# Kernel tuning notes

Hardware: AMD Instinct MI355X
Metric: run time of the kernel (lower is better)

The kernel has to match this reference:

```python
import jax, jax.numpy as jnp
import numpy as np

INPUT_SIZE = 1024
OUTPUT_SIZE = 1024
BLOCK_SIZE = 60
T = 4096
EPS = 1e-12


def setup_inputs() -> dict:
    key = jax.random.key(0)
    k1, k2, k3, k4, k5 = jax.random.split(key, 5)
    s_in = 1.0 / np.sqrt(INPUT_SIZE)
    s_out = 1.0 / np.sqrt(OUTPUT_SIZE + 2)
    return {
        "x": jax.random.normal(k1, (T, INPUT_SIZE), dtype=jnp.float32),
        "Wk": jax.random.normal(k2, (OUTPUT_SIZE, INPUT_SIZE), dtype=jnp.float32) * s_in,
        "Wq": jax.random.normal(k3, (OUTPUT_SIZE, INPUT_SIZE), dtype=jnp.float32) * s_in,
        "Wv": jax.random.normal(k4, (OUTPUT_SIZE, INPUT_SIZE), dtype=jnp.float32) * s_in,
        "Wout": jax.random.normal(k5, (INPUT_SIZE, OUTPUT_SIZE + 2), dtype=jnp.float32) * s_out,
    }


def reference(x, Wk, Wq, Wv, Wout):
    t = x.shape[0]
    # L2-normalized frame similarity / diversity  [T, T]
    x_unit = x / jnp.maximum(jnp.linalg.norm(x, axis=1, keepdims=True), EPS)
    diversity = 1.0 - x_unit @ x_unit.T

    K = x @ Wk.T
    Q = x @ Wq.T
    V = x @ Wv.T
    energies = Q @ K.T                      # [T, T]
    att_weights = jax.nn.softmax(energies, axis=-1)
    logp = jax.nn.log_softmax(energies, axis=-1)
    # normalized row entropy, then L1-normalize over T (F.normalize p=1)
    entropy = -(att_weights * logp).sum(-1) / jnp.log(jnp.float32(t))
    entropy = entropy / jnp.maximum(jnp.abs(entropy).sum(), EPS)

    # block-diagonal keep mask: same block <=> same index // block_size
    blk = jnp.arange(t) // BLOCK_SIZE
    keep = (blk[:, None] == blk[None, :]).astype(att_weights.dtype)  # [T, T]
    zero = 1.0 - keep

    att_win = att_weights * keep
    attn_rem = att_weights * zero
    div_rem = diversity * zero
    dep_factor = (div_rem * attn_rem).sum(-1) / div_rem.sum(-1)      # [T]
    # dep_factor broadcast as identical rows, masked into the kept blocks
    att_win = att_win + dep_factor[None, :] * keep

    y = att_win @ V                                                   # [T, output_size]
    characteristics = jnp.stack([entropy, dep_factor])               # [2, T] (detached in torch)
    outputs = jnp.concatenate([y, characteristics.T], axis=-1)       # [T, output_size+2]
    y_out = outputs @ Wout.T                                          # [T, input_size]
    return y_out, att_win
```

## Files before the change

### kernel.cpp

```cpp
#include <hip/hip_runtime.h>
#include <math.h>

#define T_DIM 4096
#define D_DIM 1024
#define BS 60
#define NBLK 69
#define NPART 16

typedef __attribute__((ext_vector_type(4))) float f32x4;
typedef __attribute__((ext_vector_type(8))) short short8;
#define MFMAH(a,b,c) __builtin_amdgcn_mfma_f32_16x16x32_f16((a),(b),(c),0,0,0)

static __device__ __forceinline__ ushort f2h(float f) {
  _Float16 h = (_Float16)f;
  return __builtin_bit_cast(ushort, h);
}
static __device__ __forceinline__ float h2f(ushort u) {
  _Float16 h = __builtin_bit_cast(_Float16, u);
  return (float)h;
}

__global__ __launch_bounds__(256) void k_prep(const float* __restrict__ x,
    ushort* __restrict__ xhi, ushort* __restrict__ xlo, ushort* __restrict__ u) {
  int i = blockIdx.x, tid = threadIdx.x;
  size_t off = (size_t)i * D_DIM + tid * 4;
  float4 v = *reinterpret_cast<const float4*>(x + off);
  float ss = v.x*v.x + v.y*v.y + v.z*v.z + v.w*v.w;
#pragma unroll
  for (int m = 1; m < 64; m <<= 1) ss += __shfl_xor(ss, m);
  __shared__ float sb[4];
  if ((tid & 63) == 0) sb[tid >> 6] = ss;
  __syncthreads();
  float inv = 1.0f / fmaxf(sqrtf(sb[0] + sb[1] + sb[2] + sb[3]), 1e-12f);
  ushort4 h, l, un;
  h.x = f2h(v.x); l.x = f2h(v.x - h2f(h.x)); un.x = f2h(v.x*inv);
  h.y = f2h(v.y); l.y = f2h(v.y - h2f(h.y)); un.y = f2h(v.y*inv);
  h.z = f2h(v.z); l.z = f2h(v.z - h2f(h.z)); un.z = f2h(v.z*inv);
  h.w = f2h(v.w); l.w = f2h(v.w - h2f(h.w)); un.w = f2h(v.w*inv);
  *reinterpret_cast<ushort4*>(xhi + off) = h;
  *reinterpret_cast<ushort4*>(xlo + off) = l;
  *reinterpret_cast<ushort4*>(u + off) = un;
}

__global__ __launch_bounds__(256) void k_wsplit(
    const float* __restrict__ Wq, const float* __restrict__ Wk, const float* __restrict__ Wv,
    ushort* __restrict__ Wqh, ushort* __restrict__ Wkh, ushort* __restrict__ Wvh) {
  int y = blockIdx.y;
  const float* A = (y == 0) ? Wq : (y == 1) ? Wk : Wv;
  ushort* hi = (y == 0) ? Wqh : (y == 1) ? Wkh : Wvh;
  size_t i = ((size_t)blockIdx.x * 256 + threadIdx.x) * 4;
  float4 v = *reinterpret_cast<const float4*>(A + i);
  ushort4 h;
  h.x = f2h(v.x); h.y = f2h(v.y); h.z = f2h(v.z); h.w = f2h(v.w);
  *reinterpret_cast<ushort4*>(hi + i) = h;
}

__global__ __launch_bounds__(256) void k_bsum(const ushort* __restrict__ u, float* __restrict__ Sb) {
  int b = blockIdx.x, tid = threadIdx.x;
  int j0 = b * BS;
  int w = (BS < T_DIM - j0) ? BS : (T_DIM - j0);
  int c = tid * 4;
  float4 acc = {0,0,0,0};
  for (int j = 0; j < w; ++j) {
    ushort4 v = *reinterpret_cast<const ushort4*>(u + (size_t)(j0 + j) * D_DIM + c);
    acc.x += h2f(v.x); acc.y += h2f(v.y); acc.z += h2f(v.z); acc.w += h2f(v.w);
  }
  *reinterpret_cast<float4*>(Sb + (size_t)b * D_DIM + c) = acc;
}

__global__ __launch_bounds__(256) void k_gsum(const float* __restrict__ Sb, float* __restrict__ S) {
  int c = blockIdx.x * 256 + threadIdx.x;
  float s = 0.f;
  for (int b = 0; b < NBLK; ++b) s += Sb[(size_t)b * D_DIM + c];
  S[c] = s;
}

__global__ __launch_bounds__(256,2) void k_qkv(
    const ushort* __restrict__ xhi, const ushort* __restrict__ xlo,
    const ushort* __restrict__ Wqh, const ushort* __restrict__ Wkh,
    const ushort* __restrict__ Wvh,
    ushort* __restrict__ Qhi, ushort* __restrict__ Qlo,
    ushort* __restrict__ Khi, ushort* __restrict__ Vb) {
  __shared__ __align__(16) ushort lds[28672];
  const int tid = threadIdx.x;
  const int w = tid >> 6, lane = tid & 63;
  const int wr = w >> 1, wc = w & 1;
  const int g = lane >> 4, cl = lane & 15;
  const int i0 = blockIdx.y * 128, j0 = blockIdx.x * 64;

  int adA[4], adB[2];
#pragma unroll
  for (int is = 0; is < 4; ++is) {
    int r = wr*64 + is*16 + cl;
    adA[is] = r*32 + (g ^ ((r >> 1) & 3))*8;
  }
#pragma unroll
  for (int js = 0; js < 2; ++js) {
    int r = wc*32 + js*16 + cl;
    adB[js] = r*32 + (g ^ ((r >> 1) & 3))*8;
  }
  const int ra1 = tid >> 2, ra2 = 64 + (tid >> 2), rbr = tid >> 2;
  const int sa = tid & 3;
  const int wA1 = ra1*32 + (sa ^ ((ra1 >> 1) & 3))*8;
  const int wA2 = ra2*32 + (sa ^ ((ra2 >> 1) & 3))*8;
  const int wB  = rbr*32 + (sa ^ ((rbr >> 1) & 3))*8;
  const size_t gA1 = (size_t)(i0 + ra1) * D_DIM + sa*8;
  const size_t gA2 = (size_t)(i0 + ra2) * D_DIM + sa*8;
  const size_t gB  = (size_t)(j0 + rbr) * D_DIM + sa*8;

  f32x4 accQ[4][2], accK[4][2], accV[4][2];
#pragma unroll
  for (int is = 0; is < 4; ++is)
#pragma unroll
    for (int js = 0; js < 2; ++js) {
      accQ[is][js] = (f32x4){0.f,0.f,0.f,0.f};
      accK[is][js] = (f32x4){0.f,0.f,0.f,0.f};
      accV[is][js] = (f32x4){0.f,0.f,0.f,0.f};
    }

  short8 sXh1 = *reinterpret_cast<const short8*>(xhi + gA1);
  short8 sXh2 = *reinterpret_cast<const short8*>(xhi + gA2);
  short8 sXl1 = *reinterpret_cast<const short8*>(xlo + gA1);
  short8 sXl2 = *reinterpret_cast<const short8*>(xlo + gA2);
  short8 sQh  = *reinterpret_cast<const short8*>(Wqh + gB);
  short8 sKh  = *reinterpret_cast<const short8*>(Wkh + gB);
  short8 sVh  = *reinterpret_cast<const short8*>(Wvh + gB);

  for (int ks = 0; ks < 32; ++ks) {
    const int bofs = (ks & 1) * 14336;
    *reinterpret_cast<short8*>(&lds[bofs + wA1])          = sXh1;
    *reinterpret_cast<short8*>(&lds[bofs + wA2])          = sXh2;
    *reinterpret_cast<short8*>(&lds[bofs + 4096 + wA1])   = sXl1;
    *reinterpret_cast<short8*>(&lds[bofs + 4096 + wA2])   = sXl2;
    *reinterpret_cast<short8*>(&lds[bofs + 8192 + wB])    = sQh;
    *reinterpret_cast<short8*>(&lds[bofs + 10240 + wB])   = sKh;
    *reinterpret_cast<short8*>(&lds[bofs + 12288 + wB])   = sVh;
    __syncthreads();
    short8 aH[4], aL[4], bQh[2], bKh[2], bVh[2];
#pragma unroll
    for (int is = 0; is < 4; ++is) {
      aH[is] = *reinterpret_cast<const short8*>(&lds[bofs + adA[is]]);
      aL[is] = *reinterpret_cast<const short8*>(&lds[bofs + 4096 + adA[is]]);
    }
#pragma unroll
    for (int js = 0; js < 2; ++js) {
      bQh[js] = *reinterpret_cast<const short8*>(&lds[bofs + 8192  + adB[js]]);
      bKh[js] = *reinterpret_cast<const short8*>(&lds[bofs + 10240 + adB[js]]);
      bVh[js] = *reinterpret_cast<const short8*>(&lds[bofs + 12288 + adB[js]]);
    }
    if (ks < 31) {
      const int k0 = (ks + 1) * 32;
      sXh1 = *reinterpret_cast<const short8*>(xhi + gA1 + k0);
      sXh2 = *reinterpret_cast<const short8*>(xhi + gA2 + k0);
      sXl1 = *reinterpret_cast<const short8*>(xlo + gA1 + k0);
      sXl2 = *reinterpret_cast<const short8*>(xlo + gA2 + k0);
      sQh  = *reinterpret_cast<const short8*>(Wqh + gB + k0);
      sKh  = *reinterpret_cast<const short8*>(Wkh + gB + k0);
      sVh  = *reinterpret_cast<const short8*>(Wvh + gB + k0);
    }
#pragma unroll
    for (int js = 0; js < 2; ++js)
#pragma unroll
      for (int is = 0; is < 4; ++is) {
        accQ[is][js] = MFMAH(aH[is], bQh[js], accQ[is][js]);
        accQ[is][js] = MFMAH(aL[is], bQh[js], accQ[is][js]);
        accK[is][js] = MFMAH(aH[is], bKh[js], accK[is][js]);
        accK[is][js] = MFMAH(aL[is], bKh[js], accK[is][js]);
        accV[is][js] = MFMAH(aH[is], bVh[js], accV[is][js]);
      }
  }
#pragma unroll
  for (int is = 0; is < 4; ++is)
#pragma unroll
    for (int js = 0; js < 2; ++js)
#pragma unroll
      for (int a = 0; a < 4; ++a) {
        int gi = i0 + wr*64 + is*16 + g*4 + a;
        int gj = j0 + wc*32 + js*16 + cl;
        size_t o = (size_t)gi*D_DIM + gj;
        float vq = accQ[is][js][a];
        ushort hq = f2h(vq);
        Qhi[o] = hq; Qlo[o] = f2h(vq - h2f(hq));
        Khi[o] = f2h(accK[is][js][a]);
        Vb[o]  = f2h(accV[is][js][a]);
      }
}

__global__ __launch_bounds__(256,2) void k_E(
    const ushort* __restrict__ Qhi, const ushort* __restrict__ Qlo,
    const ushort* __restrict__ Khi,
    float* __restrict__ E, float* __restrict__ pm) {
  __shared__ __align__(16) ushort lds[32768];
  __shared__ float stat_s[2][2][64];
  const int tid = threadIdx.x;
  const int bid = blockIdx.x;
  const int wg = (bid & 7) * 64 + (bid >> 3);
  const int it = wg >> 4, chunk = wg & 15;
  const int i0 = it * 128, jb = chunk * 256;
  const int w = tid >> 6, lane = tid & 63;
  const int wr = w >> 1, wc = w & 1;
  const int g = lane >> 4, cl = lane & 15;

  int adA[4], adB[8];
#pragma unroll
  for (int is = 0; is < 4; ++is) {
    int r = wr*64 + is*16 + cl;
    adA[is] = r*32 + (g ^ ((r >> 1) & 3))*8;
  }
#pragma unroll
  for (int js = 0; js < 8; ++js) {
    int r = wc*128 + js*16 + cl;
    adB[js] = 8192 + r*32 + (g ^ ((r >> 1) & 3))*8;
  }
  const int ra1 = tid >> 2, ra2 = 64 + (tid >> 2);
  const int sa = tid & 3;
  const int wA1 = ra1*32 + (sa ^ ((ra1 >> 1) & 3))*8;
  const int wA2 = ra2*32 + (sa ^ ((ra2 >> 1) & 3))*8;
  const size_t gA1 = (size_t)(i0 + ra1) * D_DIM + sa*8;
  const size_t gA2 = (size_t)(i0 + ra2) * D_DIM + sa*8;
  int wBo[4];
  size_t gBo[4];
#pragma unroll
  for (int r = 0; r < 4; ++r) {
    int rb = r*64 + (tid >> 2);
    wBo[r] = 8192 + rb*32 + (sa ^ ((rb >> 1) & 3))*8;
    gBo[r] = (size_t)(jb + rb) * D_DIM + sa*8;
  }

  f32x4 acc[4][8];
#pragma unroll
  for (int is = 0; is < 4; ++is)
#pragma unroll
    for (int js = 0; js < 8; ++js) acc[is][js] = (f32x4){0.f,0.f,0.f,0.f};

  short8 sQ1 = *reinterpret_cast<const short8*>(Qhi + gA1);
  short8 sQ2 = *reinterpret_cast<const short8*>(Qhi + gA2);
  short8 sq1 = *reinterpret_cast<const short8*>(Qlo + gA1);
  short8 sq2 = *reinterpret_cast<const short8*>(Qlo + gA2);
  short8 sK0 = *reinterpret_cast<const short8*>(Khi + gBo[0]);
  short8 sK1 = *reinterpret_cast<const short8*>(Khi + gBo[1]);
  short8 sK2 = *reinterpret_cast<const short8*>(Khi + gBo[2]);
  short8 sK3 = *reinterpret_cast<const short8*>(Khi + gBo[3]);

  for (int ks = 0; ks < 32; ++ks) {
    const int bofs = (ks & 1) * 16384;
    *reinterpret_cast<short8*>(&lds[bofs + wA1])        = sQ1;
    *reinterpret_cast<short8*>(&lds[bofs + wA2])        = sQ2;
    *reinterpret_cast<short8*>(&lds[bofs + 4096 + wA1]) = sq1;
    *reinterpret_cast<short8*>(&lds[bofs + 4096 + wA2]) = sq2;
    *reinterpret_cast<short8*>(&lds[bofs + wBo[0]])     = sK0;
    *reinterpret_cast<short8*>(&lds[bofs + wBo[1]])     = sK1;
    *reinterpret_cast<short8*>(&lds[bofs + wBo[2]])     = sK2;
    *reinterpret_cast<short8*>(&lds[bofs + wBo[3]])     = sK3;
    __syncthreads();
    short8 aQh[4], aQl[4];
#pragma unroll
    for (int is = 0; is < 4; ++is) {
      aQh[is] = *reinterpret_cast<const short8*>(&lds[bofs + adA[is]]);
      aQl[is] = *reinterpret_cast<const short8*>(&lds[bofs + 4096 + adA[is]]);
    }
    if (ks < 31) {
      const int k0 = (ks + 1) * 32;
      sQ1 = *reinterpret_cast<const short8*>(Qhi + gA1 + k0);
      sQ2 = *reinterpret_cast<const short8*>(Qhi + gA2 + k0);
      sq1 = *reinterpret_cast<const short8*>(Qlo + gA1 + k0);
      sq2 = *reinterpret_cast<const short8*>(Qlo + gA2 + k0);
      sK0 = *reinterpret_cast<const short8*>(Khi + gBo[0] + k0);
      sK1 = *reinterpret_cast<const short8*>(Khi + gBo[1] + k0);
      sK2 = *reinterpret_cast<const short8*>(Khi + gBo[2] + k0);
      sK3 = *reinterpret_cast<const short8*>(Khi + gBo[3] + k0);
    }
#pragma unroll
    for (int js = 0; js < 8; ++js) {
      short8 bK = *reinterpret_cast<const short8*>(&lds[bofs + adB[js]]);
#pragma unroll
      for (int is = 0; is < 4; ++is) {
        acc[is][js] = MFMAH(aQh[is], bK, acc[is][js]);
        acc[is][js] = MFMAH(aQl[is], bK, acc[is][js]);
      }
    }
  }
#pragma unroll
  for (int is = 0; is < 4; ++is)
#pragma unroll
    for (int a = 0; a < 4; ++a) {
      int gi = i0 + wr*64 + is*16 + g*4 + a;
      float mx = -3.0e38f;
#pragma unroll
      for (int js = 0; js < 8; ++js) {
        float e = acc[is][js][a];
        E[(size_t)gi*T_DIM + jb + wc*128 + js*16 + cl] = e;
        mx = fmaxf(mx, e);
      }
#pragma unroll
      for (int mk = 1; mk < 16; mk <<= 1) mx = fmaxf(mx, __shfl_xor(mx, mk));
      if (cl == 0) stat_s[wr][wc][is*16 + g*4 + a] = mx;
    }
  __syncthreads();
  if (tid < 128) {
    int rl = tid & 63, wr2 = tid >> 6;
    pm[(size_t)chunk*T_DIM + i0 + wr2*64 + rl] =
        fmaxf(stat_s[wr2][0][rl], stat_s[wr2][1][rl]);
  }
}

__global__ __launch_bounds__(256) void k_rowmax(const float* __restrict__ pm, float* __restrict__ mrow) {
  int i = blockIdx.x * 256 + threadIdx.x;
  float m = -3.0e38f;
  for (int c = 0; c < NPART; ++c) m = fmaxf(m, pm[(size_t)c*T_DIM + i]);
  mrow[i] = m;
}

__global__ __launch_bounds__(256,2) void k_D(
    const ushort* __restrict__ Uh, float* __restrict__ E,
    const float* __restrict__ mrow,
    float* __restrict__ eb, float* __restrict__ db,
    float* __restrict__ pZ, float* __restrict__ pWe, float* __restrict__ pWd) {
  __shared__ __align__(16) ushort lds[24576];
  __shared__ float stat_s[2][2][64][3];
  const int tid = threadIdx.x;
  const int bid = blockIdx.x;
  const int wg = (bid & 7) * 64 + (bid >> 3);
  const int it = wg >> 4, chunk = wg & 15;
  const int i0 = it * 128, jb = chunk * 256;
  const int w = tid >> 6, lane = tid & 63;
  const int wr = w >> 1, wc = w & 1;
  const int g = lane >> 4, cl = lane & 15;

  int adA[4], adB[8];
#pragma unroll
  for (int is = 0; is < 4; ++is) {
    int r = wr*64 + is*16 + cl;
    adA[is] = r*32 + (g ^ ((r >> 1) & 3))*8;
  }
#pragma unroll
  for (int js = 0; js < 8; ++js) {
    int r = wc*128 + js*16 + cl;
    adB[js] = 4096 + r*32 + (g ^ ((r >> 1) & 3))*8;
  }
  const int ra1 = tid >> 2, ra2 = 64 + (tid >> 2);
  const int sa = tid & 3;
  const int wA1 = ra1*32 + (sa ^ ((ra1 >> 1) & 3))*8;
  const int wA2 = ra2*32 + (sa ^ ((ra2 >> 1) & 3))*8;
  const size_t gA1 = (size_t)(i0 + ra1) * D_DIM + sa*8;
  const size_t gA2 = (size_t)(i0 + ra2) * D_DIM + sa*8;
  int wBo[4];
  size_t gBo[4];
#pragma unroll
  for (int r = 0; r < 4; ++r) {
    int rb = r*64 + (tid >> 2);
    wBo[r] = 4096 + rb*32 + (sa ^ ((rb >> 1) & 3))*8;
    gBo[r] = (size_t)(jb + rb) * D_DIM + sa*8;
  }

  f32x4 acc[4][8];
#pragma unroll
  for (int is = 0; is < 4; ++is)
#pragma unroll
    for (int js = 0; js < 8; ++js) acc[is][js] = (f32x4){0.f,0.f,0.f,0.f};

  short8 sU1 = *reinterpret_cast<const short8*>(Uh + gA1);
  short8 sU2 = *reinterpret_cast<const short8*>(Uh + gA2);
  short8 sV0 = *reinterpret_cast<const short8*>(Uh + gBo[0]);
  short8 sV1 = *reinterpret_cast<const short8*>(Uh + gBo[1]);
  short8 sV2 = *reinterpret_cast<const short8*>(Uh + gBo[2]);
  short8 sV3 = *reinterpret_cast<const short8*>(Uh + gBo[3]);

  for (int ks = 0; ks < 32; ++ks) {
    const int bofs = (ks & 1) * 12288;
    *reinterpret_cast<short8*>(&lds[bofs + wA1])    = sU1;
    *reinterpret_cast<short8*>(&lds[bofs + wA2])    = sU2;
    *reinterpret_cast<short8*>(&lds[bofs + wBo[0]]) = sV0;
    *reinterpret_cast<short8*>(&lds[bofs + wBo[1]]) = sV1;
    *reinterpret_cast<short8*>(&lds[bofs + wBo[2]]) = sV2;
    *reinterpret_cast<short8*>(&lds[bofs + wBo[3]]) = sV3;
    __syncthreads();
    short8 aU[4];
#pragma unroll
    for (int is = 0; is < 4; ++is)
      aU[is] = *reinterpret_cast<const short8*>(&lds[bofs + adA[is]]);
    if (ks < 31) {
      const int k0 = (ks + 1) * 32;
      sU1 = *reinterpret_cast<const short8*>(Uh + gA1 + k0);
      sU2 = *reinterpret_cast<const short8*>(Uh + gA2 + k0);
      sV0 = *reinterpret_cast<const short8*>(Uh + gBo[0] + k0);
      sV1 = *reinterpret_cast<const short8*>(Uh + gBo[1] + k0);
      sV2 = *reinterpret_cast<const short8*>(Uh + gBo[2] + k0);
      sV3 = *reinterpret_cast<const short8*>(Uh + gBo[3] + k0);
    }
#pragma unroll
    for (int js = 0; js < 8; ++js) {
      short8 bU = *reinterpret_cast<const short8*>(&lds[bofs + adB[js]]);
#pragma unroll
      for (int is = 0; is < 4; ++is)
        acc[is][js] = MFMAH(aU[is], bU, acc[is][js]);
    }
  }

  const int iw0 = i0 + wr*64;
  const int blkLo = iw0 / BS, blkHi = (iw0 + 63) / BS;
  const int jw0 = jb + wc*128;
  const bool doDiag = (jw0 < (blkHi+1)*BS) && (jw0 + 128 > blkLo*BS);

#pragma unroll
  for (int is = 0; is < 4; ++is)
#pragma unroll
    for (int a = 0; a < 4; ++a) {
      int gi = i0 + wr*64 + is*16 + g*4 + a;
      int bi = gi / BS;
      float m = mrow[gi];
      float z = 0.f, we = 0.f, wd = 0.f;
#pragma unroll
      for (int js = 0; js < 8; ++js) {
        int gj = jb + wc*128 + js*16 + cl;
        float e = E[(size_t)gi*T_DIM + gj];
        float d = acc[is][js][a];
        float p = __expf(e - m);
        z += p; we += p*e; wd += p*d;
        if (doDiag && gj / BS == bi) {
          int c = gj - bi * BS;
          eb[(size_t)gi*64 + c] = e;
          db[(size_t)gi*64 + c] = d;
        }
      }
#pragma unroll
      for (int mk = 1; mk < 16; mk <<= 1) {
        z += __shfl_xor(z, mk); we += __shfl_xor(we, mk); wd += __shfl_xor(wd, mk);
      }
      if (cl == 0) {
        int rl = is*16 + g*4 + a;
        stat_s[wr][wc][rl][0] = z;
        stat_s[wr][wc][rl][1] = we;
        stat_s[wr][wc][rl][2] = wd;
      }
    }
  __syncthreads();
  if (tid < 128) {
    int rl = tid & 63, wr2 = tid >> 6;
    size_t idx = (size_t)chunk*T_DIM + i0 + wr2*64 + rl;
    pZ[idx]  = stat_s[wr2][0][rl][0] + stat_s[wr2][1][rl][0];
    pWe[idx] = stat_s[wr2][0][rl][1] + stat_s[wr2][1][rl][1];
    pWd[idx] = stat_s[wr2][0][rl][2] + stat_s[wr2][1][rl][2];
  }
  const int zrow_ = tid >> 6;
  const int zcol  = (tid & 63) * 4;
#pragma unroll
  for (int r = 0; r < 128; r += 4)
    *reinterpret_cast<float4*>(&E[(size_t)(i0 + r + zrow_) * T_DIM + jb + zcol]) =
        (float4){0.f, 0.f, 0.f, 0.f};
}

__global__ __launch_bounds__(256) void k_merge(const float* __restrict__ pZ,
    const float* __restrict__ pWe, const float* __restrict__ pWd,
    const float* __restrict__ mrow,
    const ushort* __restrict__ Uh, const float* __restrict__ Sg, const float* __restrict__ Sb,
    const float* __restrict__ eb, const float* __restrict__ db,
    float* __restrict__ dep, float* __restrict__ ent, float* __restrict__ zrow) {
  int i = blockIdx.x, tid = threadIdx.x;
  float m = mrow[i];
  float Z = 0.f, We = 0.f, Wd = 0.f;
  for (int c = 0; c < NPART; ++c) {
    Z  += pZ [(size_t)c*T_DIM + i];
    We += pWe[(size_t)c*T_DIM + i];
    Wd += pWd[(size_t)c*T_DIM + i];
  }
  int b = i / BS, j0 = b * BS;
  int w = (BS < T_DIM - j0) ? BS : (T_DIM - j0);
  ushort4 uv = *reinterpret_cast<const ushort4*>(Uh + (size_t)i*D_DIM + tid*4);
  float4 Sv  = *reinterpret_cast<const float4*>(Sg + tid*4);
  float4 Sbv = *reinterpret_cast<const float4*>(Sb + (size_t)b*D_DIM + tid*4);
  float ux = h2f(uv.x), uy = h2f(uv.y), uz = h2f(uv.z), uw = h2f(uv.w);
  float dS  = ux*Sv.x  + uy*Sv.y  + uz*Sv.z  + uw*Sv.w;
  float dSb = ux*Sbv.x + uy*Sbv.y + uz*Sbv.z + uw*Sbv.w;
  float pb = 0.f, pdb = 0.f;
  if (tid < w) {
    float e = eb[(size_t)i*64 + tid], d = db[(size_t)i*64 + tid];
    float p = __expf(e - m);
    pb = p; pdb = p * d;
  }
  float v0 = dS, v1 = dSb, v2 = pb, v3 = pdb;
#pragma unroll
  for (int mk = 1; mk < 64; mk <<= 1) {
    v0 += __shfl_xor(v0, mk); v1 += __shfl_xor(v1, mk);
    v2 += __shfl_xor(v2, mk); v3 += __shfl_xor(v3, mk);
  }
  __shared__ float red[4][4];
  if ((tid & 63) == 0) { int wv = tid >> 6; red[0][wv]=v0; red[1][wv]=v1; red[2][wv]=v2; red[3][wv]=v3; }
  __syncthreads();
  if (tid == 0) {
    float tdS  = red[0][0]+red[0][1]+red[0][2]+red[0][3];
    float tdSb = red[1][0]+red[1][1]+red[1][2]+red[1][3];
    float s1   = red[2][0]+red[2][1]+red[2][2]+red[2][3];
    float s2   = red[3][0]+red[3][1]+red[3][2]+red[3][3];
    float invZ = 1.0f / Z;
    float num = (1.0f - s1*invZ) - (Wd - s2)*invZ;
    float den = (float)(T_DIM - w) - (tdS - tdSb);
    dep[i] = num / den;
    ent[i] = -(We*invZ - m - logf(Z)) / logf((float)T_DIM);
    zrow[i] = Z;
  }
}

__global__ __launch_bounds__(256) void k_entnorm(float* __restrict__ ent) {
  int tid = threadIdx.x;
  float s = 0.f;
  for (int i = tid; i < T_DIM; i += 256) s += fabsf(ent[i]);
#pragma unroll
  for (int mk = 1; mk < 64; mk <<= 1) s += __shfl_xor(s, mk);
  __shared__ float sb[4];
  if ((tid & 63) == 0) sb[tid >> 6] = s;
  __syncthreads();
  float inv = 1.0f / fmaxf(sb[0] + sb[1] + sb[2] + sb[3], 1e-12f);
  for (int i = tid; i < T_DIM; i += 256) ent[i] *= inv;
}

__global__ __launch_bounds__(256) void k_repack(const float* __restrict__ Wout, ushort* __restrict__ Wob) {
  int o = blockIdx.x;
  for (int k = threadIdx.x; k < 1024; k += 256)
    Wob[(size_t)o * 1024 + k] = f2h(Wout[(size_t)o * 1026 + k]);
}

__global__ __launch_bounds__(256) void k_atty(const float* __restrict__ eb, const float* __restrict__ mrow,
    const float* __restrict__ zrow, const float* __restrict__ dep, const ushort* __restrict__ Vb,
    float* __restrict__ att, ushort* __restrict__ Ybf) {
  const int b  = blockIdx.x;
  const int cc = blockIdx.y & 3, rt = blockIdx.y >> 2;
  const int j0 = b * BS;
  const int w  = (BS < T_DIM - j0) ? BS : (T_DIM - j0);
  const int r0 = rt * 12;
  __shared__ float wl[12][BS + 1];
  __shared__ __align__(16) ushort vs[BS][256];
  const int tid = threadIdx.x;
  for (int idx = tid; idx < 12 * w; idx += 256) {
    int rr = idx / w, c = idx - rr * w;
    float val = 0.f;
    if (r0 + rr < w) {
      int gi = j0 + r0 + rr;
      val = __expf(eb[(size_t)gi * 64 + c] - mrow[gi]) / zrow[gi] + dep[j0 + c];
      if (cc == 0) att[(size_t)gi * T_DIM + j0 + c] = val;
    }
    wl[rr][c] = val;
  }
  const int ccol = cc * 256;
  for (int idx = tid; idx < w * 32; idx += 256) {
    int j = idx >> 5, s = idx & 31;
    *reinterpret_cast<short8*>(&vs[j][s * 8]) =
        *reinterpret_cast<const short8*>(&Vb[(size_t)(j0 + j) * D_DIM + ccol + s * 8]);
  }
  __syncthreads();
  float acc[12];
#pragma unroll
  for (int rr = 0; rr < 12; ++rr) acc[rr] = 0.f;
  for (int j = 0; j < w; ++j) {
    float v = h2f(vs[j][tid]);
#pragma unroll
    for (int rr = 0; rr < 12; ++rr)
      acc[rr] = fmaf(wl[rr][j], v, acc[rr]);
  }
#pragma unroll
  for (int rr = 0; rr < 12; ++rr)
    if (r0 + rr < w)
      Ybf[(size_t)(j0 + r0 + rr) * D_DIM + ccol + tid] = f2h(acc[rr]);
}

__global__ __launch_bounds__(256,4) void k_final(
    const ushort* __restrict__ Ybf, const ushort* __restrict__ Wob,
    const float* __restrict__ Wout, const float* __restrict__ ent,
    const float* __restrict__ dep, float* __restrict__ yout) {
  __shared__ ushort ldsB[8192];
  const int tid = threadIdx.x;
  const int w = tid >> 6, lane = tid & 63;
  const int wr = w >> 1, wc = w & 1;
  const int g = lane >> 4, cl = lane & 15;
  const int i0 = blockIdx.y * 64, j0 = blockIdx.x * 64;
  f32x4 acc[2][2];
#pragma unroll
  for (int a = 0; a < 2; ++a)
#pragma unroll
    for (int b = 0; b < 2; ++b) acc[a][b] = (f32x4){0.f,0.f,0.f,0.f};
  const int ar0 = i0 + wr*32 + cl;

  const int r1 = tid >> 3, c1 = tid & 7;
  const int r2 = (tid + 256) >> 3, c2 = (tid + 256) & 7;
  const int lo1 = r1*64 + (c1 ^ (r1 & 7))*8;
  const int lo2 = r2*64 + (c2 ^ (r2 & 7))*8;
  const size_t gB1 = (size_t)(j0 + r1) * D_DIM + c1*8;
  const size_t gB2 = (size_t)(j0 + r2) * D_DIM + c2*8;

  short8 sB1 = *reinterpret_cast<const short8*>(Wob + gB1);
  short8 sB2 = *reinterpret_cast<const short8*>(Wob + gB2);
  short8 aY[2][2];
#pragma unroll
  for (int is = 0; is < 2; ++is)
#pragma unroll
    for (int h = 0; h < 2; ++h)
      aY[is][h] = *reinterpret_cast<const short8*>(Ybf + (size_t)(ar0 + is*16) * D_DIM + (h*4+g)*8);

  for (int ks = 0; ks < 16; ++ks) {
    const int bofs = (ks & 1) * 4096;
    *reinterpret_cast<short8*>(&ldsB[bofs + lo1]) = sB1;
    *reinterpret_cast<short8*>(&ldsB[bofs + lo2]) = sB2;
    __syncthreads();
    short8 aC[2][2];
#pragma unroll
    for (int is = 0; is < 2; ++is)
#pragma unroll
      for (int h = 0; h < 2; ++h) aC[is][h] = aY[is][h];
    if (ks < 15) {
      const int k0 = (ks + 1) * 64;
      sB1 = *reinterpret_cast<const short8*>(Wob + gB1 + k0);
      sB2 = *reinterpret_cast<const short8*>(Wob + gB2 + k0);
#pragma unroll
      for (int is = 0; is < 2; ++is)
#pragma unroll
        for (int h = 0; h < 2; ++h)
          aY[is][h] = *reinterpret_cast<const short8*>(Ybf + (size_t)(ar0 + is*16) * D_DIM + k0 + (h*4+g)*8);
    }
#pragma unroll
    for (int h = 0; h < 2; ++h)
#pragma unroll
      for (int js = 0; js < 2; ++js) {
        const int br = wc*32 + js*16 + cl;
        short8 bW = *reinterpret_cast<const short8*>(&ldsB[bofs + br*64 + ((h*4+g) ^ (br & 7))*8]);
#pragma unroll
        for (int is = 0; is < 2; ++is)
          acc[is][js] = MFMAH(aC[is][h], bW, acc[is][js]);
      }
  }
  float w1[2], w2[2];
#pragma unroll
  for (int js = 0; js < 2; ++js) {
    int gj = j0 + wc*32 + js*16 + cl;
    w1[js] = Wout[(size_t)gj * 1026 + 1024];
    w2[js] = Wout[(size_t)gj * 1026 + 1025];
  }
#pragma unroll
  for (int is = 0; is < 2; ++is)
#pragma unroll
    for (int a = 0; a < 4; ++a) {
      int gi = i0 + wr*32 + is*16 + g*4 + a;
      float e = ent[gi], d = dep[gi];
#pragma unroll
      for (int js = 0; js < 2; ++js) {
        int gj = j0 + wc*32 + js*16 + cl;
        yout[(size_t)gi * D_DIM + gj] = acc[is][js][a] + e * w1[js] + d * w2[js];
      }
    }
}

extern "C" void kernel_launch(void* const* d_in, const int* in_sizes, int n_in,
                              void* d_out, int out_size, void* d_ws, size_t ws_size,
                              hipStream_t stream) {
  const float* x    = (const float*)d_in[0];
  const float* Wk   = (const float*)d_in[1];
  const float* Wq   = (const float*)d_in[2];
  const float* Wv   = (const float*)d_in[3];
  const float* Wout = (const float*)d_in[4];
  float* out = (float*)d_out;
  char* wsb  = (char*)d_ws;

  ushort* Uh   = (ushort*)(wsb + 0);
  ushort* Vb   = (ushort*)(wsb + 8388608);
  ushort* Wqh  = (ushort*)(wsb + 16777216);
  ushort* Wkh  = (ushort*)(wsb + 18874368);
  ushort* Wvh  = (ushort*)(wsb + 20971520);
  ushort* Ybf  = (ushort*)(wsb + 23068672);
  ushort* Wob  = (ushort*)(wsb + 31457280);
  ushort* Khi  = (ushort*)(wsb + 33554432);
  ushort* xhi  = (ushort*)(wsb + 41943040);
  ushort* xlo  = (ushort*)(wsb + 50331648);
  float*  eb   = (float*)(wsb + 41943040);
  float*  db   = (float*)(wsb + 42991616);
  float*  pZ   = (float*)(wsb + 44040192);
  float*  pWe  = (float*)(wsb + 44564480);
  float*  pWd  = (float*)(wsb + 45088768);
  float*  pm   = (float*)(wsb + 45613056);
  float*  Sb   = (float*)(wsb + 46137344);
  float*  Sg   = (float*)(wsb + 46428160);
  float*  mrow = (float*)(wsb + 46432256);
  float*  zrow = (float*)(wsb + 46448640);
  float*  ent  = (float*)(wsb + 46465024);
  float*  dep  = (float*)(wsb + 46481408);

  float* yout = out;
  float* att  = out + (size_t)T_DIM * D_DIM;
  ushort* Qhi = (ushort*)yout;
  ushort* Qlo = Qhi + 4194304;
  float*  E   = att;

  k_prep<<<T_DIM, 256, 0, stream>>>(x, xhi, xlo, Uh);
  k_wsplit<<<dim3(1024, 3), 256, 0, stream>>>(Wq, Wk, Wv, Wqh, Wkh, Wvh);
  k_qkv<<<dim3(16, 32), 256, 0, stream>>>(xhi, xlo, Wqh, Wkh, Wvh,
                                          Qhi, Qlo, Khi, Vb);
  k_bsum<<<NBLK, 256, 0, stream>>>(Uh, Sb);
  k_gsum<<<4, 256, 0, stream>>>(Sb, Sg);

  k_E<<<512, 256, 0, stream>>>(Qhi, Qlo, Khi, E, pm);
  k_rowmax<<<16, 256, 0, stream>>>(pm, mrow);
  k_D<<<512, 256, 0, stream>>>(Uh, E, mrow, eb, db, pZ, pWe, pWd);
  k_merge<<<T_DIM, 256, 0, stream>>>(pZ, pWe, pWd, mrow, Uh, Sg, Sb, eb, db, dep, ent, zrow);
  k_entnorm<<<1, 256, 0, stream>>>(ent);

  k_repack<<<1024, 256, 0, stream>>>(Wout, Wob);
  k_atty<<<dim3(NBLK, 20), 256, 0, stream>>>(eb, mrow, zrow, dep, Vb, att, Ybf);
  k_final<<<dim3(16, 64), 256, 0, stream>>>(Ybf, Wob, Wout, ent, dep, yout);
}
```

Before: 293.9 us.

## Fuse energy and diversity GEMMs with online softmax partial stats

Merges the Q·K energy GEMM, the row-max pass and the U·U diversity GEMM into one kernel. Each workgroup computes local per-tile max, Z, We and Wd, and the merge kernel combines them with online-softmax rescaling. This removes the 64 MB float energy matrix write and read-back and one kernel launch. In exchange, LDS double buffering is dropped, each block runs two 128-column subtiles (reloading the Q, Qlo and U rows for each), and NPART doubles so the merge does more work.

New measurement: 392.0 us. 1.33x slower.

```diff
diff --git a/kernel.cpp b/kernel.cpp
--- a/kernel.cpp
+++ b/kernel.cpp
@@ -5,7 +5,7 @@
 #define D_DIM 1024
 #define BS 60
 #define NBLK 69
-#define NPART 16
+#define NPART 32
 
 typedef __attribute__((ext_vector_type(4))) float f32x4;
 typedef __attribute__((ext_vector_type(8))) short short8;
@@ -186,12 +186,15 @@
       }
 }
 
-__global__ __launch_bounds__(256,2) void k_E(
+__global__ __launch_bounds__(256,2) void k_ED(
     const ushort* __restrict__ Qhi, const ushort* __restrict__ Qlo,
-    const ushort* __restrict__ Khi,
-    float* __restrict__ E, float* __restrict__ pm) {
-  __shared__ __align__(16) ushort lds[32768];
-  __shared__ float stat_s[2][2][64];
+    const ushort* __restrict__ Khi, const ushort* __restrict__ Uh,
+    float* __restrict__ att,
+    float* __restrict__ eb, float* __restrict__ db,
+    float* __restrict__ pm, float* __restrict__ pZ,
+    float* __restrict__ pWe, float* __restrict__ pWd) {
+  __shared__ __align__(16) ushort lds[20480];
+  __shared__ float stat_s[2][2][64][4];
   const int tid = threadIdx.x;
   const int bid = blockIdx.x;
   const int wg = (bid & 7) * 64 + (bid >> 3);
@@ -201,16 +204,16 @@
   const int wr = w >> 1, wc = w & 1;
   const int g = lane >> 4, cl = lane & 15;
 
-  int adA[4], adB[8];
+  int adA[4], adB[4];
 #pragma unroll
   for (int is = 0; is < 4; ++is) {
     int r = wr*64 + is*16 + cl;
     adA[is] = r*32 + (g ^ ((r >> 1) & 3))*8;
   }
 #pragma unroll
-  for (int js = 0; js < 8; ++js) {
-    int r = wc*128 + js*16 + cl;
-    adB[js] = 8192 + r*32 + (g ^ ((r >> 1) & 3))*8;
+  for (int js = 0; js < 4; ++js) {
+    int r = wc*64 + js*16 + cl;
+    adB[js] = r*32 + (g ^ ((r >> 1) & 3))*8;
   }
   const int ra1 = tid >> 2, ra2 = 64 + (tid >> 2);
   const int sa = tid & 3;
@@ -218,251 +221,165 @@
   const int wA2 = ra2*32 + (sa ^ ((ra2 >> 1) & 3))*8;
   const size_t gA1 = (size_t)(i0 + ra1) * D_DIM + sa*8;
   const size_t gA2 = (size_t)(i0 + ra2) * D_DIM + sa*8;
-  int wBo[4];
-  size_t gBo[4];
-#pragma unroll
-  for (int r = 0; r < 4; ++r) {
-    int rb = r*64 + (tid >> 2);
-    wBo[r] = 8192 + rb*32 + (sa ^ ((rb >> 1) & 3))*8;
-    gBo[r] = (size_t)(jb + rb) * D_DIM + sa*8;
-  }
-
-  f32x4 acc[4][8];
-#pragma unroll
-  for (int is = 0; is < 4; ++is)
-#pragma unroll
-    for (int js = 0; js < 8; ++js) acc[is][js] = (f32x4){0.f,0.f,0.f,0.f};
-
-  short8 sQ1 = *reinterpret_cast<const short8*>(Qhi + gA1);
-  short8 sQ2 = *reinterpret_cast<const short8*>(Qhi + gA2);
-  short8 sq1 = *reinterpret_cast<const short8*>(Qlo + gA1);
-  short8 sq2 = *reinterpret_cast<const short8*>(Qlo + gA2);
-  short8 sK0 = *reinterpret_cast<const short8*>(Khi + gBo[0]);
-  short8 sK1 = *reinterpret_cast<const short8*>(Khi + gBo[1]);
-  short8 sK2 = *reinterpret_cast<const short8*>(Khi + gBo[2]);
-  short8 sK3 = *reinterpret_cast<const short8*>(Khi + gBo[3]);
-
-  for (int ks = 0; ks < 32; ++ks) {
-    const int bofs = (ks & 1) * 16384;
-    *reinterpret_cast<short8*>(&lds[bofs + wA1])        = sQ1;
-    *reinterpret_cast<short8*>(&lds[bofs + wA2])        = sQ2;
-    *reinterpret_cast<short8*>(&lds[bofs + 4096 + wA1]) = sq1;
-    *reinterpret_cast<short8*>(&lds[bofs + 4096 + wA2]) = sq2;
-    *reinterpret_cast<short8*>(&lds[bofs + wBo[0]])     = sK0;
-    *reinterpret_cast<short8*>(&lds[bofs + wBo[1]])     = sK1;
-    *reinterpret_cast<short8*>(&lds[bofs + wBo[2]])     = sK2;
-    *reinterpret_cast<short8*>(&lds[bofs + wBo[3]])     = sK3;
-    __syncthreads();
-    short8 aQh[4], aQl[4];
-#pragma unroll
-    for (int is = 0; is < 4; ++is) {
-      aQh[is] = *reinterpret_cast<const short8*>(&lds[bofs + adA[is]]);
-      aQl[is] = *reinterpret_cast<const short8*>(&lds[bofs + 4096 + adA[is]]);
-    }
-    if (ks < 31) {
-      const int k0 = (ks + 1) * 32;
-      sQ1 = *reinterpret_cast<const short8*>(Qhi + gA1 + k0);
-      sQ2 = *reinterpret_cast<const short8*>(Qhi + gA2 + k0);
-      sq1 = *reinterpret_cast<const short8*>(Qlo + gA1 + k0);
-      sq2 = *reinterpret_cast<const short8*>(Qlo + gA2 + k0);
-      sK0 = *reinterpret_cast<const short8*>(Khi + gBo[0] + k0);
-      sK1 = *reinterpret_cast<const short8*>(Khi + gBo[1] + k0);
-      sK2 = *reinterpret_cast<const short8*>(Khi + gBo[2] + k0);
-      sK3 = *reinterpret_cast<const short8*>(Khi + gBo[3] + k0);
-    }
-#pragma unroll
-    for (int js = 0; js < 8; ++js) {
-      short8 bK = *reinterpret_cast<const short8*>(&lds[bofs + adB[js]]);
-#pragma unroll
-      for (int is = 0; is < 4; ++is) {
-        acc[is][js] = MFMAH(aQh[is], bK, acc[is][js]);
-        acc[is][js] = MFMAH(aQl[is], bK, acc[is][js]);
-      }
-    }
-  }
-#pragma unroll
-  for (int is = 0; is < 4; ++is)
-#pragma unroll
-    for (int a = 0; a < 4; ++a) {
-      int gi = i0 + wr*64 + is*16 + g*4 + a;
-      float mx = -3.0e38f;
-#pragma unroll
-      for (int js = 0; js < 8; ++js) {
-        float e = acc[is][js][a];
-        E[(size_t)gi*T_DIM + jb + wc*128 + js*16 + cl] = e;
-        mx = fmaxf(mx, e);
-      }
-#pragma unroll
-      for (int mk = 1; mk < 16; mk <<= 1) mx = fmaxf(mx, __shfl_xor(mx, mk));
-      if (cl == 0) stat_s[wr][wc][is*16 + g*4 + a] = mx;
-    }
-  __syncthreads();
-  if (tid < 128) {
-    int rl = tid & 63, wr2 = tid >> 6;
-    pm[(size_t)chunk*T_DIM + i0 + wr2*64 + rl] =
-        fmaxf(stat_s[wr2][0][rl], stat_s[wr2][1][rl]);
-  }
-}
-
-__global__ __launch_bounds__(256) void k_rowmax(const float* __restrict__ pm, float* __restrict__ mrow) {
-  int i = blockIdx.x * 256 + threadIdx.x;
-  float m = -3.0e38f;
-  for (int c = 0; c < NPART; ++c) m = fmaxf(m, pm[(size_t)c*T_DIM + i]);
-  mrow[i] = m;
-}
-
-__global__ __launch_bounds__(256,2) void k_D(
-    const ushort* __restrict__ Uh, float* __restrict__ E,
-    const float* __restrict__ mrow,
-    float* __restrict__ eb, float* __restrict__ db,
-    float* __restrict__ pZ, float* __restrict__ pWe, float* __restrict__ pWd) {
-  __shared__ __align__(16) ushort lds[24576];
-  __shared__ float stat_s[2][2][64][3];
-  const int tid = threadIdx.x;
-  const int bid = blockIdx.x;
-  const int wg = (bid & 7) * 64 + (bid >> 3);
-  const int it = wg >> 4, chunk = wg & 15;
-  const int i0 = it * 128, jb = chunk * 256;
-  const int w = tid >> 6, lane = tid & 63;
-  const int wr = w >> 1, wc = w & 1;
-  const int g = lane >> 4, cl = lane & 15;
-
-  int adA[4], adB[8];
-#pragma unroll
-  for (int is = 0; is < 4; ++is) {
-    int r = wr*64 + is*16 + cl;
-    adA[is] = r*32 + (g ^ ((r >> 1) & 3))*8;
-  }
-#pragma unroll
-  for (int js = 0; js < 8; ++js) {
-    int r = wc*128 + js*16 + cl;
-    adB[js] = 4096 + r*32 + (g ^ ((r >> 1) & 3))*8;
-  }
-  const int ra1 = tid >> 2, ra2 = 64 + (tid >> 2);
-  const int sa = tid & 3;
-  const int wA1 = ra1*32 + (sa ^ ((ra1 >> 1) & 3))*8;
-  const int wA2 = ra2*32 + (sa ^ ((ra2 >> 1) & 3))*8;
-  const size_t gA1 = (size_t)(i0 + ra1) * D_DIM + sa*8;
-  const size_t gA2 = (size_t)(i0 + ra2) * D_DIM + sa*8;
-  int wBo[4];
-  size_t gBo[4];
-#pragma unroll
-  for (int r = 0; r < 4; ++r) {
-    int rb = r*64 + (tid >> 2);
-    wBo[r] = 4096 + rb*32 + (sa ^ ((rb >> 1) & 3))*8;
-    gBo[r] = (size_t)(jb + rb) * D_DIM + sa*8;
-  }
-
-  f32x4 acc[4][8];
-#pragma unroll
-  for (int is = 0; is < 4; ++is)
-#pragma unroll
-    for (int js = 0; js < 8; ++js) acc[is][js] = (f32x4){0.f,0.f,0.f,0.f};
-
-  short8 sU1 = *reinterpret_cast<const short8*>(Uh + gA1);
-  short8 sU2 = *reinterpret_cast<const short8*>(Uh + gA2);
-  short8 sV0 = *reinterpret_cast<const short8*>(Uh + gBo[0]);
-  short8 sV1 = *reinterpret_cast<const short8*>(Uh + gBo[1]);
-  short8 sV2 = *reinterpret_cast<const short8*>(Uh + gBo[2]);
-  short8 sV3 = *reinterpret_cast<const short8*>(Uh + gBo[3]);
-
-  for (int ks = 0; ks < 32; ++ks) {
-    const int bofs = (ks & 1) * 12288;
-    *reinterpret_cast<short8*>(&lds[bofs + wA1])    = sU1;
-    *reinterpret_cast<short8*>(&lds[bofs + wA2])    = sU2;
-    *reinterpret_cast<short8*>(&lds[bofs + wBo[0]]) = sV0;
-    *reinterpret_cast<short8*>(&lds[bofs + wBo[1]]) = sV1;
-    *reinterpret_cast<short8*>(&lds[bofs + wBo[2]]) = sV2;
-    *reinterpret_cast<short8*>(&lds[bofs + wBo[3]]) = sV3;
-    __syncthreads();
-    short8 aU[4];
-#pragma unroll
-    for (int is = 0; is < 4; ++is)
-      aU[is] = *reinterpret_cast<const short8*>(&lds[bofs + adA[is]]);
-    if (ks < 31) {
-      const int k0 = (ks + 1) * 32;
-      sU1 = *reinterpret_cast<const short8*>(Uh + gA1 + k0);
-      sU2 = *reinterpret_cast<const short8*>(Uh + gA2 + k0);
-      sV0 = *reinterpret_cast<const short8*>(Uh + gBo[0] + k0);
-      sV1 = *reinterpret_cast<const short8*>(Uh + gBo[1] + k0);
-      sV2 = *reinterpret_cast<const short8*>(Uh + gBo[2] + k0);
-      sV3 = *reinterpret_cast<const short8*>(Uh + gBo[3] + k0);
-    }
-#pragma unroll
-    for (int js = 0; js < 8; ++js) {
-      short8 bU = *reinterpret_cast<const short8*>(&lds[bofs + adB[js]]);
-#pragma unroll
-      for (int is = 0; is < 4; ++is)
-        acc[is][js] = MFMAH(aU[is], bU, acc[is][js]);
-    }
-  }
 
   const int iw0 = i0 + wr*64;
   const int blkLo = iw0 / BS, blkHi = (iw0 + 63) / BS;
-  const int jw0 = jb + wc*128;
-  const bool doDiag = (jw0 < (blkHi+1)*BS) && (jw0 + 128 > blkLo*BS);
-
-#pragma unroll
-  for (int is = 0; is < 4; ++is)
-#pragma unroll
-    for (int a = 0; a < 4; ++a) {
-      int gi = i0 + wr*64 + is*16 + g*4 + a;
-      int bi = gi / BS;
-      float m = mrow[gi];
-      float z = 0.f, we = 0.f, wd = 0.f;
-#pragma unroll
-      for (int js = 0; js < 8; ++js) {
-        int gj = jb + wc*128 + js*16 + cl;
-        float e = E[(size_t)gi*T_DIM + gj];
-        float d = acc[is][js][a];
-        float p = __expf(e - m);
-        z += p; we += p*e; wd += p*d;
-        if (doDiag && gj / BS == bi) {
-          int c = gj - bi * BS;
-          eb[(size_t)gi*64 + c] = e;
-          db[(size_t)gi*64 + c] = d;
+
+  for (int jt = 0; jt < 2; ++jt) {
+    const int jb2 = jb + jt * 128;
+    const size_t gB1 = (size_t)(jb2 + ra1) * D_DIM + sa*8;
+    const size_t gB2 = (size_t)(jb2 + ra2) * D_DIM + sa*8;
+
+    f32x4 accE[4][4], accD[4][4];
+#pragma unroll
+    for (int is = 0; is < 4; ++is)
+#pragma unroll
+      for (int js = 0; js < 4; ++js) {
+        accE[is][js] = (f32x4){0.f,0.f,0.f,0.f};
+        accD[is][js] = (f32x4){0.f,0.f,0.f,0.f};
+      }
+
+    short8 sQ1 = *reinterpret_cast<const short8*>(Qhi + gA1);
+    short8 sQ2 = *reinterpret_cast<const short8*>(Qhi + gA2);
+    short8 sq1 = *reinterpret_cast<const short8*>(Qlo + gA1);
+    short8 sq2 = *reinterpret_cast<const short8*>(Qlo + gA2);
+    short8 sU1 = *reinterpret_cast<const short8*>(Uh + gA1);
+    short8 sU2 = *reinterpret_cast<const short8*>(Uh + gA2);
+    short8 sK1 = *reinterpret_cast<const short8*>(Khi + gB1);
+    short8 sK2 = *reinterpret_cast<const short8*>(Khi + gB2);
+    short8 sV1 = *reinterpret_cast<const short8*>(Uh + gB1);
+    short8 sV2 = *reinterpret_cast<const short8*>(Uh + gB2);
+
+    for (int ks = 0; ks < 32; ++ks) {
+      __syncthreads();
+      *reinterpret_cast<short8*>(&lds[wA1])          = sQ1;
+      *reinterpret_cast<short8*>(&lds[wA2])          = sQ2;
+      *reinterpret_cast<short8*>(&lds[4096 + wA1])   = sq1;
+      *reinterpret_cast<short8*>(&lds[4096 + wA2])   = sq2;
+      *reinterpret_cast<short8*>(&lds[8192 + wA1])   = sU1;
+      *reinterpret_cast<short8*>(&lds[8192 + wA2])   = sU2;
+      *reinterpret_cast<short8*>(&lds[12288 + wA1])  = sK1;
+      *reinterpret_cast<short8*>(&lds[12288 + wA2])  = sK2;
+      *reinterpret_cast<short8*>(&lds[16384 + wA1])  = sV1;
+      *reinterpret_cast<short8*>(&lds[16384 + wA2])  = sV2;
+      __syncthreads();
+      short8 aQh[4], aQl[4], aU[4];
+#pragma unroll
+      for (int is = 0; is < 4; ++is) {
+        aQh[is] = *reinterpret_cast<const short8*>(&lds[adA[is]]);
+        aQl[is] = *reinterpret_cast<const short8*>(&lds[4096 + adA[is]]);
+        aU [is] = *reinterpret_cast<const short8*>(&lds[8192 + adA[is]]);
+      }
+      if (ks < 31) {
+        const int k0 = (ks + 1) * 32;
+        sQ1 = *reinterpret_cast<const short8*>(Qhi + gA1 + k0);
+        sQ2 = *reinterpret_cast<const short8*>(Qhi + gA2 + k0);
+        sq1 = *reinterpret_cast<const short8*>(Qlo + gA1 + k0);
+        sq2 = *reinterpret_cast<const short8*>(Qlo + gA2 + k0);
+        sU1 = *reinterpret_cast<const short8*>(Uh + gA1 + k0);
+        sU2 = *reinterpret_cast<const short8*>(Uh + gA2 + k0);
+        sK1 = *reinterpret_cast<const short8*>(Khi + gB1 + k0);
+        sK2 = *reinterpret_cast<const short8*>(Khi + gB2 + k0);
+        sV1 = *reinterpret_cast<const short8*>(Uh + gB1 + k0);
+        sV2 = *reinterpret_cast<const short8*>(Uh + gB2 + k0);
+      }
+#pragma unroll
+      for (int js = 0; js < 4; ++js) {
+        short8 bK = *reinterpret_cast<const short8*>(&lds[12288 + adB[js]]);
+        short8 bU = *reinterpret_cast<const short8*>(&lds[16384 + adB[js]]);
+#pragma unroll
+        for (int is = 0; is < 4; ++is) {
+          accE[is][js] = MFMAH(aQh[is], bK, accE[is][js]);
+          accE[is][js] = MFMAH(aQl[is], bK, accE[is][js]);
+          accD[is][js] = MFMAH(aU[is],  bU, accD[is][js]);
         }
       }
-#pragma unroll
-      for (int mk = 1; mk < 16; mk <<= 1) {
-        z += __shfl_xor(z, mk); we += __shfl_xor(we, mk); wd += __shfl_xor(wd, mk);
-      }
-      if (cl == 0) {
-        int rl = is*16 + g*4 + a;
-        stat_s[wr][wc][rl][0] = z;
-        stat_s[wr][wc][rl][1] = we;
-        stat_s[wr][wc][rl][2] = wd;
-      }
-    }
-  __syncthreads();
-  if (tid < 128) {
-    int rl = tid & 63, wr2 = tid >> 6;
-    size_t idx = (size_t)chunk*T_DIM + i0 + wr2*64 + rl;
-    pZ[idx]  = stat_s[wr2][0][rl][0] + stat_s[wr2][1][rl][0];
-    pWe[idx] = stat_s[wr2][0][rl][1] + stat_s[wr2][1][rl][1];
-    pWd[idx] = stat_s[wr2][0][rl][2] + stat_s[wr2][1][rl][2];
+    }
+
+    const int jw0 = jb2 + wc*64;
+    const bool doDiag = (jw0 < (blkHi+1)*BS) && (jw0 + 64 > blkLo*BS);
+#pragma unroll
+    for (int is = 0; is < 4; ++is)
+#pragma unroll
+      for (int a = 0; a < 4; ++a) {
+        int gi = i0 + wr*64 + is*16 + g*4 + a;
+        int bi = gi / BS;
+        float e0 = accE[is][0][a], e1 = accE[is][1][a];
+        float e2 = accE[is][2][a], e3 = accE[is][3][a];
+        float d0 = accD[is][0][a], d1 = accD[is][1][a];
+        float d2 = accD[is][2][a], d3 = accD[is][3][a];
+        if (doDiag) {
+#pragma unroll
+          for (int js = 0; js < 4; ++js) {
+            int gj = jw0 + js*16 + cl;
+            if (gj / BS == bi) {
+              int c = gj - bi * BS;
+              float e = (js == 0) ? e0 : (js == 1) ? e1 : (js == 2) ? e2 : e3;
+              float d = (js == 0) ? d0 : (js == 1) ? d1 : (js == 2) ? d2 : d3;
+              eb[(size_t)gi*64 + c] = e;
+              db[(size_t)gi*64 + c] = d;
+            }
+          }
+        }
+        float tmax = fmaxf(fmaxf(e0, e1), fmaxf(e2, e3));
+#pragma unroll
+        for (int mk = 1; mk < 16; mk <<= 1) tmax = fmaxf(tmax, __shfl_xor(tmax, mk));
+        float p0 = __expf(e0 - tmax), p1 = __expf(e1 - tmax);
+        float p2 = __expf(e2 - tmax), p3 = __expf(e3 - tmax);
+        float z  = p0 + p1 + p2 + p3;
+        float we = p0*e0 + p1*e1 + p2*e2 + p3*e3;
+        float wd = p0*d0 + p1*d1 + p2*d2 + p3*d3;
+#pragma unroll
+        for (int mk = 1; mk < 16; mk <<= 1) {
+          z += __shfl_xor(z, mk); we += __shfl_xor(we, mk); wd += __shfl_xor(wd, mk);
+        }
+        if (cl == 0) {
+          int rl = is*16 + g*4 + a;
+          stat_s[wr][wc][rl][0] = tmax;
+          stat_s[wr][wc][rl][1] = z;
+          stat_s[wr][wc][rl][2] = we;
+          stat_s[wr][wc][rl][3] = wd;
+        }
+      }
+    __syncthreads();
+    if (tid < 128) {
+      int rl = tid & 63, wr2 = tid >> 6;
+      float m0 = stat_s[wr2][0][rl][0], Z0 = stat_s[wr2][0][rl][1];
+      float We0 = stat_s[wr2][0][rl][2], Wd0 = stat_s[wr2][0][rl][3];
+      float m1 = stat_s[wr2][1][rl][0], Z1 = stat_s[wr2][1][rl][1];
+      float We1 = stat_s[wr2][1][rl][2], Wd1 = stat_s[wr2][1][rl][3];
+      float nm = fmaxf(m0, m1);
+      float s0 = __expf(m0 - nm), s1 = __expf(m1 - nm);
+      size_t idx = (size_t)(chunk*2 + jt) * T_DIM + i0 + wr2*64 + rl;
+      pm[idx]  = nm;
+      pZ[idx]  = Z0*s0 + Z1*s1;
+      pWe[idx] = We0*s0 + We1*s1;
+      pWd[idx] = Wd0*s0 + Wd1*s1;
+    }
+    __syncthreads();
   }
   const int zrow_ = tid >> 6;
   const int zcol  = (tid & 63) * 4;
 #pragma unroll
   for (int r = 0; r < 128; r += 4)
-    *reinterpret_cast<float4*>(&E[(size_t)(i0 + r + zrow_) * T_DIM + jb + zcol]) =
+    *reinterpret_cast<float4*>(&att[(size_t)(i0 + r + zrow_) * T_DIM + jb + zcol]) =
         (float4){0.f, 0.f, 0.f, 0.f};
 }
 
-__global__ __launch_bounds__(256) void k_merge(const float* __restrict__ pZ,
-    const float* __restrict__ pWe, const float* __restrict__ pWd,
-    const float* __restrict__ mrow,
+__global__ __launch_bounds__(256) void k_merge(const float* __restrict__ pm,
+    const float* __restrict__ pZ, const float* __restrict__ pWe, const float* __restrict__ pWd,
     const ushort* __restrict__ Uh, const float* __restrict__ Sg, const float* __restrict__ Sb,
     const float* __restrict__ eb, const float* __restrict__ db,
-    float* __restrict__ dep, float* __restrict__ ent, float* __restrict__ zrow) {
+    float* __restrict__ dep, float* __restrict__ ent,
+    float* __restrict__ mrow, float* __restrict__ zrow) {
   int i = blockIdx.x, tid = threadIdx.x;
-  float m = mrow[i];
-  float Z = 0.f, We = 0.f, Wd = 0.f;
-  for (int c = 0; c < NPART; ++c) {
-    Z  += pZ [(size_t)c*T_DIM + i];
-    We += pWe[(size_t)c*T_DIM + i];
-    Wd += pWd[(size_t)c*T_DIM + i];
+  float m = pm[i], Z = pZ[i], We = pWe[i], Wd = pWd[i];
+  for (int c = 1; c < NPART; ++c) {
+    float om = pm[(size_t)c*T_DIM + i], oZ = pZ[(size_t)c*T_DIM + i];
+    float oWe = pWe[(size_t)c*T_DIM + i], oWd = pWd[(size_t)c*T_DIM + i];
+    float nm = fmaxf(m, om);
+    float s1 = __expf(m - nm), s2 = __expf(om - nm);
+    Z = Z*s1 + oZ*s2; We = We*s1 + oWe*s2; Wd = Wd*s1 + oWd*s2; m = nm;
   }
   int b = i / BS, j0 = b * BS;
   int w = (BS < T_DIM - j0) ? BS : (T_DIM - j0);
@@ -497,7 +414,7 @@
     float den = (float)(T_DIM - w) - (tdS - tdSb);
     dep[i] = num / den;
     ent[i] = -(We*invZ - m - logf(Z)) / logf((float)T_DIM);
-    zrow[i] = Z;
+    mrow[i] = m; zrow[i] = Z;
   }
 }
 
@@ -686,7 +603,6 @@
   float* att  = out + (size_t)T_DIM * D_DIM;
   ushort* Qhi = (ushort*)yout;
   ushort* Qlo = Qhi + 4194304;
-  float*  E   = att;
 
   k_prep<<<T_DIM, 256, 0, stream>>>(x, xhi, xlo, Uh);
   k_wsplit<<<dim3(1024, 3), 256, 0, stream>>>(Wq, Wk, Wv, Wqh, Wkh, Wvh);
@@ -695,10 +611,8 @@
   k_bsum<<<NBLK, 256, 0, stream>>>(Uh, Sb);
   k_gsum<<<4, 256, 0, stream>>>(Sb, Sg);
 
-  k_E<<<512, 256, 0, stream>>>(Qhi, Qlo, Khi, E, pm);
-  k_rowmax<<<16, 256, 0, stream>>>(pm, mrow);
-  k_D<<<512, 256, 0, stream>>>(Uh, E, mrow, eb, db, pZ, pWe, pWd);
-  k_merge<<<T_DIM, 256, 0, stream>>>(pZ, pWe, pWd, mrow, Uh, Sg, Sb, eb, db, dep, ent, zrow);
+  k_ED<<<512, 256, 0, stream>>>(Qhi, Qlo, Khi, Uh, att, eb, db, pm, pZ, pWe, pWd);
+  k_merge<<<T_DIM, 256, 0, stream>>>(pm, pZ, pWe, pWd, Uh, Sg, Sb, eb, db, dep, ent, mrow, zrow);
   k_entnorm<<<1, 256, 0, stream>>>(ent);
 
   k_repack<<<1024, 256, 0, stream>>>(Wout, Wob);
```
